# Kernel tuning notes

Hardware: AMD Instinct MI355X
Metric: run time of the kernel (lower is better)

## Reference

```python
import jax, jax.numpy as jnp
import numpy as np

B, T, HID = 8, 1024, 1024
N_HEADS, HEAD = 16, HID // 16
MAX_F, BASE = 1024, 10000.0


def _rope_tables():
    inv_freq = 1.0 / (BASE ** (np.arange(0, HEAD, 2, dtype=np.float32) / HEAD))
    t = np.arange(MAX_F, dtype=np.float32)
    freqs = np.einsum('i,j->ij', t, inv_freq)  # (MAX_F, HEAD/2)
    emb = np.concatenate([freqs, freqs], axis=-1)  # (MAX_F, HEAD)
    return jnp.asarray(np.cos(emb)), jnp.asarray(np.sin(emb))


def setup_inputs() -> dict:
    key = jax.random.key(0)
    ks = jax.random.split(key, 6)
    x = jax.random.normal(ks[0], (B, T, HID), dtype=jnp.float32)
    Wq = jax.random.normal(ks[1], (HID, HID), dtype=jnp.float32) * 0.02
    Wk = jax.random.normal(ks[2], (HID, HID), dtype=jnp.float32) * 0.02
    Wv = jax.random.normal(ks[3], (HID, HID), dtype=jnp.float32) * 0.02
    Wo = jax.random.normal(ks[4], (HID, HID), dtype=jnp.float32) * 0.02
    cos, sin = _rope_tables()
    attn_mask = jnp.ones((B, T, T), dtype=jnp.int32)
    timestamp = jax.random.randint(ks[5], (B, T), 0, MAX_F, dtype=jnp.int32)
    return {"x": x, "Wq": Wq, "Wk": Wk, "Wv": Wv, "Wo": Wo,
            "cos": cos, "sin": sin, "attn_mask": attn_mask, "timestamp": timestamp}


def _rotate_half(u):
    u1, u2 = u[..., : HEAD // 2], u[..., HEAD // 2:]
    return jnp.concatenate([-u2, u1], axis=-1)


def reference(x, Wq, Wk, Wv, Wo, cos, sin, attn_mask, timestamp):
    Bx, Tx, _ = x.shape
    # QKV projections (nn.Linear: x @ W.T), reshape to (B, H, T, head)
    def proj(W):
        return (x @ W.T).reshape(Bx, Tx, N_HEADS, HEAD).transpose(0, 2, 1, 3)
    q, k, v = proj(Wq), proj(Wk), proj(Wv)
    # RoPE: gather cos/sin by timestamp, broadcast over heads (unsqueeze dim 1)
    c = cos[timestamp][:, None]  # (B, 1, T, head)
    s = sin[timestamp][:, None]
    q = q * c + _rotate_half(q) * s
    k = k * c + _rotate_half(k) * s
    # Masked SDPA
    scale = 1.0 / jnp.sqrt(jnp.float32(HEAD))
    scores = jnp.einsum('bhqd,bhkd->bhqk', q, k) * scale
    mask = attn_mask[:, None].astype(bool)  # (B, 1, T, T) broadcasts over heads
    scores = jnp.where(mask, scores, jnp.finfo(scores.dtype).min)
    attn = jax.nn.softmax(scores, axis=-1)
    out = jnp.einsum('bhqk,bhkd->bhqd', attn, v)
    out = out.transpose(0, 2, 1, 3).reshape(Bx, Tx, HID)
    return out @ Wo.T
```

## Files before the change

kernel.cpp:

```cpp
#include <hip/hip_runtime.h>
#include <hip/hip_bf16.h>

#define B_   8
#define T_   1024
#define HID_ 1024
#define NH_  16
#define HD_  64
#define K2   2048

typedef __attribute__((ext_vector_type(8))) short bf16x8;
typedef __attribute__((ext_vector_type(4))) float f32x4;

__device__ __forceinline__ void gl_lds16(const void* g, void* l) {
    __builtin_amdgcn_global_load_lds((const __attribute__((address_space(1))) void*)g,
                                     (__attribute__((address_space(3))) void*)l, 16, 0, 0);
}

__device__ __forceinline__ float fast_exp2(float x) {
    return __builtin_amdgcn_exp2f(x);
}

__global__ __launch_bounds__(256) void cast_bf16(const float* __restrict__ X,
                                                 __hip_bfloat16* __restrict__ Y) {
    int gid = blockIdx.x * 256 + threadIdx.x;
    int f = gid << 2;
    float4 xv = *(const float4*)(X + f);
    union { __hip_bfloat16 b[4]; ushort4 u; } p;
    p.b[0] = __float2bfloat16(xv.x);
    p.b[1] = __float2bfloat16(xv.y);
    p.b[2] = __float2bfloat16(xv.z);
    p.b[3] = __float2bfloat16(xv.w);
    *(ushort4*)(Y + f) = p.u;
}

__global__ __launch_bounds__(256) void dup_bf16_w(const float* __restrict__ X,
                                                  __hip_bfloat16* __restrict__ Y) {
    int gid = blockIdx.x * 256 + threadIdx.x;
    int f = gid << 2;
    int m = f >> 10, kk = f & 1023;
    float4 xv = *(const float4*)(X + f);
    union { __hip_bfloat16 b[4]; ushort4 u; } ph;
    ph.b[0] = __float2bfloat16(xv.x);
    ph.b[1] = __float2bfloat16(xv.y);
    ph.b[2] = __float2bfloat16(xv.z);
    ph.b[3] = __float2bfloat16(xv.w);
    size_t base = (size_t)m * K2 + kk;
    *(ushort4*)(Y + base) = ph.u;
    *(ushort4*)(Y + base + 1024) = ph.u;
}

__global__ __launch_bounds__(256) void mask_pack(const int* __restrict__ mask,
                                                 unsigned long long* __restrict__ mbits) {
    int gid = blockIdx.x * 256 + threadIdx.x;
    int wid = gid >> 6;
    int lane = threadIdx.x & 63;
    int m = mask[(size_t)wid * 64 + lane];
    unsigned long long bal = __ballot(m != 0);
    if (lane == 0) mbits[wid] = bal;
}

__global__ __launch_bounds__(256) void mask_dense(const unsigned long long* __restrict__ mbits,
                                                  unsigned int* __restrict__ tdense) {
    int gid = blockIdx.x * 256 + threadIdx.x;
    int e = gid >> 6;
    int lane = threadIdx.x & 63;
    int b = e >> 8, qt = (e >> 4) & 15, kt = e & 15;
    unsigned long long val = mbits[((size_t)(b * T_ + qt * 64 + lane)) * 16 + kt];
    unsigned long long bal = __ballot(val == ~0ull);
    if (lane == 0) tdense[e] = (bal == ~0ull) ? 1u : 0u;
}

template<int MODE, int KD>
__global__ __launch_bounds__(256, 4) void gemm_mfma(const __hip_bfloat16* __restrict__ A,
                                                    const __hip_bfloat16* __restrict__ Wp,
                                                    float* __restrict__ C0,
                                                    __hip_bfloat16* __restrict__ qbf,
                                                    __hip_bfloat16* __restrict__ kbf,
                                                    __hip_bfloat16* __restrict__ vt,
                                                    const float* __restrict__ cost,
                                                    const float* __restrict__ sint,
                                                    const int* __restrict__ ts) {
    __shared__ __hip_bfloat16 As[2][128 * 32];
    __shared__ __hip_bfloat16 Bs[2][128 * 32];
    const int tid = threadIdx.x;
    const int lane = tid & 63;
    const int w = tid >> 6;
    const int wm = w >> 1, wn = w & 1;
    const int m0 = blockIdx.y * 128, n0 = blockIdx.x * 128;
    const int r0 = tid >> 2;
    const int ks = (tid & 3) << 3;
    const int ml = lane & 15;
    const int kg = (lane >> 4) << 3;
    const int q4 = (lane >> 4) << 2;

    f32x4 acc[4][4];
#pragma unroll
    for (int i = 0; i < 4; ++i)
#pragma unroll
        for (int j = 0; j < 4; ++j) acc[i][j] = (f32x4){0.f, 0.f, 0.f, 0.f};

    for (int k0 = 0; k0 < KD; k0 += 64) {
#pragma unroll
        for (int c = 0; c < 2; ++c) {
            const int kc = k0 + c * 32 + ks;
            gl_lds16(A  + (size_t)(m0 + r0)      * KD + kc, &As[c][r0 * 32 + ks]);
            gl_lds16(A  + (size_t)(m0 + 64 + r0) * KD + kc, &As[c][(64 + r0) * 32 + ks]);
            gl_lds16(Wp + (size_t)(n0 + r0)      * KD + kc, &Bs[c][r0 * 32 + ks]);
            gl_lds16(Wp + (size_t)(n0 + 64 + r0) * KD + kc, &Bs[c][(64 + r0) * 32 + ks]);
        }
        __syncthreads();

#pragma unroll
        for (int c = 0; c < 2; ++c) {
            bf16x8 a[4], b[4];
#pragma unroll
            for (int mi = 0; mi < 4; ++mi)
                a[mi] = *(const bf16x8*)(&As[c][(wm * 64 + mi * 16 + ml) * 32 + kg]);
#pragma unroll
            for (int ni = 0; ni < 4; ++ni)
                b[ni] = *(const bf16x8*)(&Bs[c][(wn * 64 + ni * 16 + ml) * 32 + kg]);
#pragma unroll
            for (int mi = 0; mi < 4; ++mi)
#pragma unroll
                for (int ni = 0; ni < 4; ++ni)
                    acc[mi][ni] = __builtin_amdgcn_mfma_f32_16x16x32_bf16(a[mi], b[ni], acc[mi][ni], 0, 0, 0);
        }
        __syncthreads();
    }

    if (MODE == 0) {
#pragma unroll
        for (int mi = 0; mi < 4; ++mi)
#pragma unroll
            for (int ni = 0; ni < 4; ++ni) {
                int n = n0 + wn * 64 + ni * 16 + ml;
#pragma unroll
                for (int r = 0; r < 4; ++r) {
                    int m = m0 + wm * 64 + mi * 16 + q4 + r;
                    C0[(size_t)m * 1024 + n] = acc[mi][ni][r];
                }
            }
    } else {
        const int nB = n0 + wn * 64;
        const int sel = nB >> 10;
        const int h = (nB & 1023) >> 6;
        if (sel < 2) {
            __hip_bfloat16* dst = sel ? kbf : qbf;
#pragma unroll
            for (int mi = 0; mi < 4; ++mi) {
#pragma unroll
                for (int r = 0; r < 4; ++r) {
                    int m = m0 + wm * 64 + mi * 16 + q4 + r;
                    int tsv = ts[m];
                    int bb = m >> 10, t = m & 1023;
                    size_t rowoff = ((size_t)(bb * NH_ + h) * T_ + t) * HD_;
#pragma unroll
                    for (int ni = 0; ni < 4; ++ni) {
                        int d = ni * 16 + ml;
                        float c = cost[tsv * HD_ + d];
                        float s = sint[tsv * HD_ + d];
                        float u  = acc[mi][ni][r];
                        float up = acc[mi][ni ^ 2][r];
                        float o = (ni < 2) ? (u * c - up * s) : (u * c + up * s);
                        dst[rowoff + d] = __float2bfloat16(o);
                    }
                }
            }
        } else {
#pragma unroll
            for (int mi = 0; mi < 4; ++mi)
#pragma unroll
                for (int r = 0; r < 4; ++r) {
                    int m = m0 + wm * 64 + mi * 16 + q4 + r;
                    int bb = m >> 10, t = m & 1023;
#pragma unroll
                    for (int ni = 0; ni < 4; ++ni) {
                        int d = ni * 16 + ml;
                        vt[((size_t)(bb * NH_ + h) * HD_ + d) * T_ + t] =
                            __float2bfloat16(acc[mi][ni][r]);
                    }
                }
        }
    }
}

__global__ __launch_bounds__(256) void flash_mfma(const __hip_bfloat16* __restrict__ qg,
                                                  const __hip_bfloat16* __restrict__ kg_,
                                                  const __hip_bfloat16* __restrict__ vtg,
                                                  const unsigned long long* __restrict__ mbits,
                                                  const unsigned int* __restrict__ tdense,
                                                  __hip_bfloat16* __restrict__ xs) {
    __shared__ __hip_bfloat16 Ks[2][64 * 72];
    __shared__ __hip_bfloat16 Vt[2][64 * 72];
    __shared__ __hip_bfloat16 Ps[64 * 72];
    const int id = blockIdx.x;
    const int qt = (id >> 3) & 15;
    const int hb = ((id >> 7) << 3) | (id & 7);
    const int h = hb & 15, b = hb >> 4;
    const int tid = threadIdx.x;
    const int lane = tid & 63;
    const int w = tid >> 6;
    const int ml = lane & 15;
    const int kg8 = (lane >> 4) << 3;
    const int q4 = (lane >> 4) << 2;
    const int q0 = qt * 64;
    const size_t bh_off = (size_t)(b * NH_ + h) * T_ * HD_;
    const __hip_bfloat16* qb = qg + bh_off;
    const __hip_bfloat16* kb = kg_ + bh_off;
    const __hip_bfloat16* vtb = vtg + bh_off;
    const float SCL = 0.125f * 1.44269504f;

    bf16x8 qf0 = *(const bf16x8*)(qb + (size_t)(q0 + w * 16 + ml) * HD_ + kg8);
    bf16x8 qf1 = *(const bf16x8*)(qb + (size_t)(q0 + w * 16 + ml) * HD_ + 32 + kg8);

    f32x4 acc_o[4];
    float lp[4] = {0.f, 0.f, 0.f, 0.f};
#pragma unroll
    for (int i = 0; i < 4; ++i) acc_o[i] = (f32x4){0.f, 0.f, 0.f, 0.f};

#pragma unroll
    for (int p = 0; p < 2; ++p) {
        int fidx = tid + p * 256;
        int rr = fidx >> 3, c8 = (fidx & 7) << 3;
        *(bf16x8*)(&Ks[0][rr * 72 + c8]) = *(const bf16x8*)(kb + (size_t)rr * HD_ + c8);
        *(bf16x8*)(&Vt[0][rr * 72 + c8]) = *(const bf16x8*)(vtb + (size_t)rr * T_ + c8);
    }

    for (int kt = 0; kt < 16; ++kt) {
        const int cur = kt & 1;
        __syncthreads();
        if (kt < 15) {
            const int k0n = (kt + 1) * 64;
            const int nb = cur ^ 1;
#pragma unroll
            for (int p = 0; p < 2; ++p) {
                int fidx = tid + p * 256;
                int rr = fidx >> 3, c8 = (fidx & 7) << 3;
                *(bf16x8*)(&Ks[nb][rr * 72 + c8]) = *(const bf16x8*)(kb + (size_t)(k0n + rr) * HD_ + c8);
                *(bf16x8*)(&Vt[nb][rr * 72 + c8]) = *(const bf16x8*)(vtb + (size_t)rr * T_ + k0n + c8);
            }
        }

        f32x4 sacc[4];
#pragma unroll
        for (int ni = 0; ni < 4; ++ni) sacc[ni] = (f32x4){0.f, 0.f, 0.f, 0.f};
#pragma unroll
        for (int ni = 0; ni < 4; ++ni) {
            bf16x8 kf0 = *(const bf16x8*)(&Ks[cur][(ni * 16 + ml) * 72 + kg8]);
            bf16x8 kf1 = *(const bf16x8*)(&Ks[cur][(ni * 16 + ml) * 72 + 32 + kg8]);
            sacc[ni] = __builtin_amdgcn_mfma_f32_16x16x32_bf16(qf0, kf0, sacc[ni], 0, 0, 0);
            sacc[ni] = __builtin_amdgcn_mfma_f32_16x16x32_bf16(qf1, kf1, sacc[ni], 0, 0, 0);
        }

        if (tdense[(b * 16 + qt) * 16 + kt]) {
#pragma unroll
            for (int r = 0; r < 4; ++r) {
                float pv[4];
#pragma unroll
                for (int ni = 0; ni < 4; ++ni) pv[ni] = fast_exp2(sacc[ni][r] * SCL);
                lp[r] += (pv[0] + pv[1]) + (pv[2] + pv[3]);
#pragma unroll
                for (int ni = 0; ni < 4; ++ni)
                    Ps[(w * 16 + q4 + r) * 72 + ni * 16 + ml] = __float2bfloat16(pv[ni]);
            }
        } else {
            unsigned long long mb[4];
#pragma unroll
            for (int r = 0; r < 4; ++r)
                mb[r] = mbits[((size_t)(b * T_ + q0 + w * 16 + q4 + r)) * 16 + kt];
#pragma unroll
            for (int r = 0; r < 4; ++r) {
                float pv[4];
#pragma unroll
                for (int ni = 0; ni < 4; ++ni) {
                    bool on = (mb[r] >> (ni * 16 + ml)) & 1ull;
                    pv[ni] = on ? fast_exp2(sacc[ni][r] * SCL) : 0.f;
                }
                lp[r] += (pv[0] + pv[1]) + (pv[2] + pv[3]);
#pragma unroll
                for (int ni = 0; ni < 4; ++ni)
                    Ps[(w * 16 + q4 + r) * 72 + ni * 16 + ml] = __float2bfloat16(pv[ni]);
            }
        }

        bf16x8 pf0 = *(const bf16x8*)(Ps + (w * 16 + ml) * 72 + kg8);
        bf16x8 pf1 = *(const bf16x8*)(Ps + (w * 16 + ml) * 72 + 32 + kg8);
#pragma unroll
        for (int dt = 0; dt < 4; ++dt) {
            bf16x8 vf0 = *(const bf16x8*)(&Vt[cur][(dt * 16 + ml) * 72 + kg8]);
            bf16x8 vf1 = *(const bf16x8*)(&Vt[cur][(dt * 16 + ml) * 72 + 32 + kg8]);
            acc_o[dt] = __builtin_amdgcn_mfma_f32_16x16x32_bf16(pf0, vf0, acc_o[dt], 0, 0, 0);
            acc_o[dt] = __builtin_amdgcn_mfma_f32_16x16x32_bf16(pf1, vf1, acc_o[dt], 0, 0, 0);
        }
    }

#pragma unroll
    for (int r = 0; r < 4; ++r) {
        float l = lp[r];
#pragma unroll
        for (int off = 1; off < 16; off <<= 1)
            l += __shfl_xor(l, off, 16);
        float inv = 1.0f / l;
        size_t rb = (size_t)(b * T_ + q0 + w * 16 + q4 + r) * K2;
#pragma unroll
        for (int dt = 0; dt < 4; ++dt) {
            float val = acc_o[dt][r] * inv;
            int col = h * HD_ + dt * 16 + ml;
            __hip_bfloat16 hi = __float2bfloat16(val);
            __hip_bfloat16 lo = __float2bfloat16(val - __bfloat162float(hi));
            xs[rb + col] = hi;
            xs[rb + 1024 + col] = lo;
        }
    }
}

extern "C" void kernel_launch(void* const* d_in, const int* in_sizes, int n_in,
                              void* d_out, int out_size, void* d_ws, size_t ws_size,
                              hipStream_t stream) {
    const float* x    = (const float*)d_in[0];
    const float* Wq   = (const float*)d_in[1];
    const float* Wk   = (const float*)d_in[2];
    const float* Wv   = (const float*)d_in[3];
    const float* Wo   = (const float*)d_in[4];
    const float* cost = (const float*)d_in[5];
    const float* sint = (const float*)d_in[6];
    const int*   mask = (const int*)d_in[7];
    const int*   ts   = (const int*)d_in[8];
    float* out = (float*)d_out;

    const size_t MB = 1ull << 20;
    char* wsp = (char*)d_ws;
    __hip_bfloat16* qbf  = (__hip_bfloat16*)(wsp + 0 * MB);
    __hip_bfloat16* kbf  = (__hip_bfloat16*)(wsp + 16 * MB);
    __hip_bfloat16* vt   = (__hip_bfloat16*)(wsp + 32 * MB);
    __hip_bfloat16* xs   = (__hip_bfloat16*)(wsp + 48 * MB);
    __hip_bfloat16* xb   = (__hip_bfloat16*)(wsp + 80 * MB);
    __hip_bfloat16* wqkv = (__hip_bfloat16*)(wsp + 96 * MB);
    __hip_bfloat16* wo   = (__hip_bfloat16*)(wsp + 102 * MB);
    unsigned long long* mbits = (unsigned long long*)(wsp + 106 * MB);
    unsigned int* tdense = (unsigned int*)(wsp + 107 * MB);

    cast_bf16<<<8192, 256, 0, stream>>>(x, xb);
    cast_bf16<<<1024, 256, 0, stream>>>(Wq, wqkv);
    cast_bf16<<<1024, 256, 0, stream>>>(Wk, wqkv + (size_t)1024 * 1024);
    cast_bf16<<<1024, 256, 0, stream>>>(Wv, wqkv + (size_t)2048 * 1024);
    dup_bf16_w<<<1024, 256, 0, stream>>>(Wo, wo);
    mask_pack<<<32768, 256, 0, stream>>>(mask, mbits);
    mask_dense<<<512, 256, 0, stream>>>(mbits, tdense);

    gemm_mfma<2, 1024><<<dim3(24, 64), 256, 0, stream>>>(xb, wqkv, nullptr,
                                                         qbf, kbf, vt, cost, sint, ts);

    flash_mfma<<<2048, 256, 0, stream>>>(qbf, kbf, vt, mbits, tdense, xs);

    gemm_mfma<0, K2><<<dim3(8, 64), 256, 0, stream>>>(xs, wo, out,
                                                      nullptr, nullptr, nullptr,
                                                      nullptr, nullptr, nullptr);
}
```

Baseline: 333.8 us.

## Use async global-to-LDS loads with XOR-swizzled tiles and transposed score MFMA

Replaces register-staged K/V tile copies with global_load_lds direct-to-LDS transfers into unpadded, XOR-swizzled 64-wide tiles, shrinking LDS use. It swaps the operands of the QK^T MFMA so each lane holds scores for one query row, which lets the mask be a single 64-bit word per lane. P is written to a per-wave swizzled buffer as packed 8-byte stores, and the row-sum reduction becomes two shuffles instead of four. It also adds an occupancy hint of 4 blocks per SM. The swizzle and direct-load addressing must line up exactly with the MFMA fragment layout, or the results will be wrong.

```diff
diff --git a/kernel.cpp b/kernel.cpp
--- a/kernel.cpp
+++ b/kernel.cpp
@@ -184,15 +184,15 @@
     }
 }
 
-__global__ __launch_bounds__(256) void flash_mfma(const __hip_bfloat16* __restrict__ qg,
-                                                  const __hip_bfloat16* __restrict__ kg_,
-                                                  const __hip_bfloat16* __restrict__ vtg,
-                                                  const unsigned long long* __restrict__ mbits,
-                                                  const unsigned int* __restrict__ tdense,
-                                                  __hip_bfloat16* __restrict__ xs) {
-    __shared__ __hip_bfloat16 Ks[2][64 * 72];
-    __shared__ __hip_bfloat16 Vt[2][64 * 72];
-    __shared__ __hip_bfloat16 Ps[64 * 72];
+__global__ __launch_bounds__(256, 4) void flash_mfma(const __hip_bfloat16* __restrict__ qg,
+                                                     const __hip_bfloat16* __restrict__ kg_,
+                                                     const __hip_bfloat16* __restrict__ vtg,
+                                                     const unsigned long long* __restrict__ mbits,
+                                                     const unsigned int* __restrict__ tdense,
+                                                     __hip_bfloat16* __restrict__ xs) {
+    __shared__ __hip_bfloat16 Ks[2][64 * 64];
+    __shared__ __hip_bfloat16 Vt[2][64 * 64];
+    __shared__ __hip_bfloat16 Ps[4][16 * 64];
     const int id = blockIdx.x;
     const int qt = (id >> 3) & 15;
     const int hb = ((id >> 7) << 3) | (id & 7);
@@ -201,8 +201,9 @@
     const int lane = tid & 63;
     const int w = tid >> 6;
     const int ml = lane & 15;
-    const int kg8 = (lane >> 4) << 3;
-    const int q4 = (lane >> 4) << 2;
+    const int g4 = lane >> 4;
+    const int kg8 = g4 << 3;
+    const int q4 = g4 << 2;
     const int q0 = qt * 64;
     const size_t bh_off = (size_t)(b * NH_ + h) * T_ * HD_;
     const __hip_bfloat16* qb = qg + bh_off;
@@ -210,20 +211,25 @@
     const __hip_bfloat16* vtb = vtg + bh_off;
     const float SCL = 0.125f * 1.44269504f;
 
+    const int srow = lane >> 3;
+    const int sg8 = ((lane & 7) ^ srow) << 3;
+    const int sx = ((g4 ^ (ml & 7)) << 4);
+    const int pswz = (ml & 7) << 4;
+
     bf16x8 qf0 = *(const bf16x8*)(qb + (size_t)(q0 + w * 16 + ml) * HD_ + kg8);
     bf16x8 qf1 = *(const bf16x8*)(qb + (size_t)(q0 + w * 16 + ml) * HD_ + 32 + kg8);
 
     f32x4 acc_o[4];
-    float lp[4] = {0.f, 0.f, 0.f, 0.f};
+    float lsum = 0.f;
 #pragma unroll
     for (int i = 0; i < 4; ++i) acc_o[i] = (f32x4){0.f, 0.f, 0.f, 0.f};
+    char* psw = (char*)&Ps[w][0];
 
 #pragma unroll
     for (int p = 0; p < 2; ++p) {
-        int fidx = tid + p * 256;
-        int rr = fidx >> 3, c8 = (fidx & 7) << 3;
-        *(bf16x8*)(&Ks[0][rr * 72 + c8]) = *(const bf16x8*)(kb + (size_t)rr * HD_ + c8);
-        *(bf16x8*)(&Vt[0][rr * 72 + c8]) = *(const bf16x8*)(vtb + (size_t)rr * T_ + c8);
+        const int rbase = p * 32 + w * 8;
+        gl_lds16(kb  + (size_t)(rbase + srow) * HD_ + sg8, &Ks[0][rbase * 64]);
+        gl_lds16(vtb + (size_t)(rbase + srow) * T_  + sg8, &Vt[0][rbase * 64]);
     }
 
     for (int kt = 0; kt < 16; ++kt) {
@@ -234,73 +240,66 @@
             const int nb = cur ^ 1;
 #pragma unroll
             for (int p = 0; p < 2; ++p) {
-                int fidx = tid + p * 256;
-                int rr = fidx >> 3, c8 = (fidx & 7) << 3;
-                *(bf16x8*)(&Ks[nb][rr * 72 + c8]) = *(const bf16x8*)(kb + (size_t)(k0n + rr) * HD_ + c8);
-                *(bf16x8*)(&Vt[nb][rr * 72 + c8]) = *(const bf16x8*)(vtb + (size_t)rr * T_ + k0n + c8);
+                const int rbase = p * 32 + w * 8;
+                gl_lds16(kb  + (size_t)(k0n + rbase + srow) * HD_ + sg8, &Ks[nb][rbase * 64]);
+                gl_lds16(vtb + (size_t)(rbase + srow) * T_ + k0n + sg8, &Vt[nb][rbase * 64]);
             }
         }
 
         f32x4 sacc[4];
 #pragma unroll
         for (int ni = 0; ni < 4; ++ni) sacc[ni] = (f32x4){0.f, 0.f, 0.f, 0.f};
+        const char* ksb = (const char*)&Ks[cur][0];
 #pragma unroll
         for (int ni = 0; ni < 4; ++ni) {
-            bf16x8 kf0 = *(const bf16x8*)(&Ks[cur][(ni * 16 + ml) * 72 + kg8]);
-            bf16x8 kf1 = *(const bf16x8*)(&Ks[cur][(ni * 16 + ml) * 72 + 32 + kg8]);
-            sacc[ni] = __builtin_amdgcn_mfma_f32_16x16x32_bf16(qf0, kf0, sacc[ni], 0, 0, 0);
-            sacc[ni] = __builtin_amdgcn_mfma_f32_16x16x32_bf16(qf1, kf1, sacc[ni], 0, 0, 0);
-        }
-
-        if (tdense[(b * 16 + qt) * 16 + kt]) {
+            const char* rp = ksb + (ni * 16 + ml) * 128;
+            bf16x8 kf0 = *(const bf16x8*)(rp + sx);
+            bf16x8 kf1 = *(const bf16x8*)(rp + (sx ^ 64));
+            sacc[ni] = __builtin_amdgcn_mfma_f32_16x16x32_bf16(kf0, qf0, sacc[ni], 0, 0, 0);
+            sacc[ni] = __builtin_amdgcn_mfma_f32_16x16x32_bf16(kf1, qf1, sacc[ni], 0, 0, 0);
+        }
+
+        unsigned long long mb = ~0ull;
+        if (!tdense[(b * 16 + qt) * 16 + kt])
+            mb = mbits[((size_t)(b * T_ + q0 + w * 16 + ml)) * 16 + kt];
+#pragma unroll
+        for (int ni = 0; ni < 4; ++ni) {
+            float pv[4];
 #pragma unroll
             for (int r = 0; r < 4; ++r) {
-                float pv[4];
-#pragma unroll
-                for (int ni = 0; ni < 4; ++ni) pv[ni] = fast_exp2(sacc[ni][r] * SCL);
-                lp[r] += (pv[0] + pv[1]) + (pv[2] + pv[3]);
-#pragma unroll
-                for (int ni = 0; ni < 4; ++ni)
-                    Ps[(w * 16 + q4 + r) * 72 + ni * 16 + ml] = __float2bfloat16(pv[ni]);
+                int kv = ni * 16 + q4 + r;
+                pv[r] = ((mb >> kv) & 1ull) ? fast_exp2(sacc[ni][r] * SCL) : 0.f;
+                lsum += pv[r];
             }
-        } else {
-            unsigned long long mb[4];
-#pragma unroll
-            for (int r = 0; r < 4; ++r)
-                mb[r] = mbits[((size_t)(b * T_ + q0 + w * 16 + q4 + r)) * 16 + kt];
-#pragma unroll
-            for (int r = 0; r < 4; ++r) {
-                float pv[4];
-#pragma unroll
-                for (int ni = 0; ni < 4; ++ni) {
-                    bool on = (mb[r] >> (ni * 16 + ml)) & 1ull;
-                    pv[ni] = on ? fast_exp2(sacc[ni][r] * SCL) : 0.f;
-                }
-                lp[r] += (pv[0] + pv[1]) + (pv[2] + pv[3]);
-#pragma unroll
-                for (int ni = 0; ni < 4; ++ni)
-                    Ps[(w * 16 + q4 + r) * 72 + ni * 16 + ml] = __float2bfloat16(pv[ni]);
-            }
-        }
-
-        bf16x8 pf0 = *(const bf16x8*)(Ps + (w * 16 + ml) * 72 + kg8);
-        bf16x8 pf1 = *(const bf16x8*)(Ps + (w * 16 + ml) * 72 + 32 + kg8);
+            union { __hip_bfloat16 bb[4]; unsigned long long u8; } pk;
+            pk.bb[0] = __float2bfloat16(pv[0]);
+            pk.bb[1] = __float2bfloat16(pv[1]);
+            pk.bb[2] = __float2bfloat16(pv[2]);
+            pk.bb[3] = __float2bfloat16(pv[3]);
+            *(unsigned long long*)(psw + ml * 128 + ((ni * 32 + g4 * 8) ^ pswz)) = pk.u8;
+        }
+
+        bf16x8 pf0 = *(const bf16x8*)(psw + ml * 128 + sx);
+        bf16x8 pf1 = *(const bf16x8*)(psw + ml * 128 + (sx ^ 64));
+
+        const char* vsb = (const char*)&Vt[cur][0];
 #pragma unroll
         for (int dt = 0; dt < 4; ++dt) {
-            bf16x8 vf0 = *(const bf16x8*)(&Vt[cur][(dt * 16 + ml) * 72 + kg8]);
-            bf16x8 vf1 = *(const bf16x8*)(&Vt[cur][(dt * 16 + ml) * 72 + 32 + kg8]);
+            const char* rp = vsb + (dt * 16 + ml) * 128;
+            bf16x8 vf0 = *(const bf16x8*)(rp + sx);
+            bf16x8 vf1 = *(const bf16x8*)(rp + (sx ^ 64));
             acc_o[dt] = __builtin_amdgcn_mfma_f32_16x16x32_bf16(pf0, vf0, acc_o[dt], 0, 0, 0);
             acc_o[dt] = __builtin_amdgcn_mfma_f32_16x16x32_bf16(pf1, vf1, acc_o[dt], 0, 0, 0);
         }
     }
 
+    float l = lsum;
+    l += __shfl_xor(l, 16);
+    l += __shfl_xor(l, 32);
 #pragma unroll
     for (int r = 0; r < 4; ++r) {
-        float l = lp[r];
-#pragma unroll
-        for (int off = 1; off < 16; off <<= 1)
-            l += __shfl_xor(l, off, 16);
-        float inv = 1.0f / l;
+        float lr = __shfl(l, q4 + r, 16);
+        float inv = 1.0f / lr;
         size_t rb = (size_t)(b * T_ + q0 + w * 16 + q4 + r) * K2;
 #pragma unroll
         for (int dt = 0; dt < 4; ++dt) {
```

Measured after the change: 329.6 us. About the same (-1.3%).
